# Kernel optimization log

Measured on AMD Instinct MI355X. Metric: run time of the kernel, lower is better.

The kernel has to match this reference:

```python
import jax, jax.numpy as jnp
import numpy as np

NUM_QUESTION = 10000


def setup_inputs() -> dict:
    key = jax.random.key(0)
    ks = jax.random.split(key, 12)
    B, L, DK, SLOTS = 64, 200, 128, 64
    return {
        "question_seq": jax.random.randint(ks[0], (B, L), 0, NUM_QUESTION),
        "correct_seq": jax.random.randint(ks[1], (B, L), 0, 2),
        "q_emb": jax.random.normal(ks[2], (NUM_QUESTION, DK), jnp.float32) * 0.05,
        "v_emb": jax.random.normal(ks[3], (2 * NUM_QUESTION, DK), jnp.float32) * 0.05,
        "Mk": jax.random.normal(ks[4], (SLOTS, DK), jnp.float32) * 0.1,
        "Mv0": jax.random.normal(ks[5], (SLOTS, DK), jnp.float32) * 0.1,
        "eW": jax.random.normal(ks[6], (DK, DK), jnp.float32) * 0.05,
        "eb": jnp.zeros((DK,), jnp.float32),
        "aW": jax.random.normal(ks[7], (DK, DK), jnp.float32) * 0.05,
        "ab": jnp.zeros((DK,), jnp.float32),
        "fW": jax.random.normal(ks[8], (DK, 2 * DK), jnp.float32) * 0.05,
        "fb": jnp.zeros((DK,), jnp.float32),
        "pW": jax.random.normal(ks[9], (1, DK), jnp.float32) * 0.05,
        "pb": jnp.zeros((1,), jnp.float32),
    }


def reference(question_seq, correct_seq, q_emb, v_emb, Mk, Mv0,
              eW, eb, aW, ab, fW, fb, pW, pb):
    B = question_seq.shape[0]
    x = question_seq + NUM_QUESTION * correct_seq          # [B, L]
    k = q_emb[question_seq]                                # [B, L, DK]
    v = v_emb[x]                                           # [B, L, DK]
    w = jax.nn.softmax(jnp.einsum("bld,sd->bls", k, Mk), axis=-1)  # [B, L, S]
    e = jax.nn.sigmoid(v @ eW.T + eb)                      # [B, L, DK]
    a = jnp.tanh(v @ aW.T + ab)                            # [B, L, DK]

    Mv_init = jnp.broadcast_to(Mv0[None], (B,) + Mv0.shape)  # [B, S, DK]

    def step(Mvt, inp):
        wt, et, at = inp  # [B,S], [B,DK], [B,DK]
        # read uses memory BEFORE the write (Mv[:, :-1] in the original)
        read = jnp.einsum("bs,bsd->bd", wt, Mvt)
        we = wt[:, :, None]
        Mvt = Mvt * (1.0 - we * et[:, None, :]) + we * at[:, None, :]
        return Mvt, read

    xs = (w.transpose(1, 0, 2), e.transpose(1, 0, 2), a.transpose(1, 0, 2))
    _, reads = jax.lax.scan(step, Mv_init, xs)             # reads: [L, B, DK]
    reads = reads.transpose(1, 0, 2)                       # [B, L, DK]

    f = jnp.tanh(jnp.concatenate([reads, k], axis=-1) @ fW.T + fb)
    predict_score = jax.nn.sigmoid(f @ pW.T + pb)[..., 0]  # [B, L]
    return predict_score
```

## Files before the change

kernel.cpp:

```cpp
#include <hip/hip_runtime.h>
#include <hip/hip_bf16.h>

#define NQ 10000
#define BATCH 64
#define SEQL 200
#define DKD 128
#define SLOTS 64
#define NTOK (BATCH*SEQL)

typedef __attribute__((ext_vector_type(8))) short bh8;
typedef __attribute__((ext_vector_type(4))) float f32x4;
typedef unsigned short u16;
typedef unsigned int u32;

__device__ __forceinline__ float sigmoidf_(float x){ return 1.0f/(1.0f + __expf(-x)); }
__device__ __forceinline__ float tanhf_(float x){
  float ax = fminf(fabsf(x), 30.0f);
  float t = __expf(-2.0f*ax);
  float r = (1.0f-t)/(1.0f+t);
  return copysignf(r, x);
}
__device__ __forceinline__ u16 f2b(float x){
  u32 u = __builtin_bit_cast(u32, x);
  u32 r = (u + 0x7FFFu + ((u >> 16) & 1u)) >> 16;
  return (u16)r;
}
__device__ __forceinline__ bh8 cvt8(const float* s){
  float4 v0 = *(const float4*)s, v1 = *(const float4*)(s + 4);
  bh8 h;
  h[0]=(short)f2b(v0.x); h[1]=(short)f2b(v0.y); h[2]=(short)f2b(v0.z); h[3]=(short)f2b(v0.w);
  h[4]=(short)f2b(v1.x); h[5]=(short)f2b(v1.y); h[6]=(short)f2b(v1.z); h[7]=(short)f2b(v1.w);
  return h;
}
__device__ __forceinline__ int swz(int row, int col16, int rowBytes){
  return row*rowBytes + ((col16 ^ (row & 7)) << 4);
}

__global__ __launch_bounds__(512) void wea_kernel(
    const int* __restrict__ qseq, const int* __restrict__ cseq,
    const float* __restrict__ q_emb, const float* __restrict__ v_emb,
    const float* __restrict__ Mk, const float* __restrict__ eW,
    const float* __restrict__ aW,
    const float* __restrict__ eb, const float* __restrict__ ab,
    float* __restrict__ w_out, float* __restrict__ eT, float* __restrict__ aT)
{
  __shared__ __align__(16) char smem[73728];
  char* As = smem;
  char* Bs = smem + 8192;
  float* Ls = (float*)(smem + 24576);

  const int tid = threadIdx.x;
  const int l = tid & 63, wv = tid >> 6;
  const bool isW = (blockIdx.x < 400);
  const int tok0 = (isW ? blockIdx.x : blockIdx.x - 400) * 32;

  {
    int row = tid >> 4, c16 = tid & 15;
    const float* src;
    if (isW){ int q = qseq[tok0+row]; src = q_emb + (size_t)q*DKD + c16*8; }
    else    { int x = qseq[tok0+row] + NQ*cseq[tok0+row]; src = v_emb + (size_t)x*DKD + c16*8; }
    *(bh8*)(As + swz(row, c16, 256)) = cvt8(src);
  }
  if (isW){
    #pragma unroll
    for (int m = 0; m < 2; ++m){
      int idx = tid + 512*m; int row = idx >> 4, c16 = idx & 15;
      *(bh8*)(Bs + swz(row, c16, 256)) = cvt8(Mk + (size_t)row*DKD + c16*8);
    }
  } else {
    #pragma unroll
    for (int m = 0; m < 8; ++m){
      int idx = tid + 512*m; int row = idx >> 4, c16 = idx & 15;
      const float* src = (row < 128) ? (eW + (size_t)row*DKD) : (aW + (size_t)(row-128)*DKD);
      *(bh8*)(Bs + swz(row, c16, 256)) = cvt8(src + c16*8);
    }
  }
  __syncthreads();

  if (isW){
    const int m = wv & 1, n = wv >> 1;
    f32x4 acc = {0.f,0.f,0.f,0.f};
    #pragma unroll
    for (int kc = 0; kc < 4; ++kc){
      bh8 af = *(const bh8*)(As + swz(m*16 + (l&15), kc*4 + (l>>4), 256));
      bh8 bf = *(const bh8*)(Bs + swz(n*16 + (l&15), kc*4 + (l>>4), 256));
      acc = __builtin_amdgcn_mfma_f32_16x16x32_bf16(af, bf, acc, 0, 0, 0);
    }
    #pragma unroll
    for (int r = 0; r < 4; ++r){
      int tok = m*16 + (l>>4)*4 + r, out = n*16 + (l&15);
      Ls[tok*68 + out] = acc[r];
    }
    __syncthreads();
    #pragma unroll
    for (int i = 0; i < 4; ++i){
      int tok = wv*4 + i;
      float x = Ls[tok*68 + l];
      float mx = x;
      #pragma unroll
      for (int off = 32; off >= 1; off >>= 1) mx = fmaxf(mx, __shfl_xor(mx, off));
      float p = __expf(x - mx);
      float s = p;
      #pragma unroll
      for (int off = 32; off >= 1; off >>= 1) s += __shfl_xor(s, off);
      w_out[(size_t)(tok0+tok)*SLOTS + l] = p / s;
    }
  } else {
    const int m = wv & 1, nq = (wv >> 1) * 4;
    f32x4 acc[4] = {{0.f,0.f,0.f,0.f},{0.f,0.f,0.f,0.f},{0.f,0.f,0.f,0.f},{0.f,0.f,0.f,0.f}};
    #pragma unroll
    for (int kc = 0; kc < 4; ++kc){
      bh8 af = *(const bh8*)(As + swz(m*16 + (l&15), kc*4 + (l>>4), 256));
      #pragma unroll
      for (int j = 0; j < 4; ++j){
        bh8 bf = *(const bh8*)(Bs + swz((nq+j)*16 + (l&15), kc*4 + (l>>4), 256));
        acc[j] = __builtin_amdgcn_mfma_f32_16x16x32_bf16(af, bf, acc[j], 0, 0, 0);
      }
    }
    #pragma unroll
    for (int j = 0; j < 4; ++j){
      int out = (nq+j)*16 + (l&15);
      bool is_e = (out < 128);
      int dd = out & 127;
      float bias = is_e ? eb[dd] : ab[dd];
      float4 sv;
      #pragma unroll
      for (int r = 0; r < 4; ++r){
        float xv = acc[j][r] + bias;
        ((float*)&sv)[r] = is_e ? sigmoidf_(xv) : tanhf_(xv);
      }
      int tg = tok0 + m*16 + (l>>4)*4;
      int bb = tg / SEQL, tl = tg - bb*SEQL;
      float* dst = (is_e ? eT : aT) + ((size_t)bb*DKD + dd)*SEQL + tl;
      *(float4*)dst = sv;
    }
  }
}

__device__ __forceinline__ float dpp_row_sum16(float x){
  float t;
  t = __builtin_bit_cast(float, __builtin_amdgcn_update_dpp(0, __builtin_bit_cast(int,x), 0x111, 0xf, 0xf, true)); x += t;
  t = __builtin_bit_cast(float, __builtin_amdgcn_update_dpp(0, __builtin_bit_cast(int,x), 0x112, 0xf, 0xf, true)); x += t;
  t = __builtin_bit_cast(float, __builtin_amdgcn_update_dpp(0, __builtin_bit_cast(int,x), 0x114, 0xf, 0xf, true)); x += t;
  t = __builtin_bit_cast(float, __builtin_amdgcn_update_dpp(0, __builtin_bit_cast(int,x), 0x118, 0xf, 0xf, true)); x += t;
  return x;
}

#define TCH 8
#define NCH 25

__global__ __launch_bounds__(256) void scan_kernel(
    const float* __restrict__ Mv0,
    const float* __restrict__ w_in, const float* __restrict__ eT,
    const float* __restrict__ aT, u16* __restrict__ r16)
{
  __shared__ float eaS[2][2][16][8];
  __shared__ float rbuf[2][TCH][16];
  const int tid = threadIdx.x;
  const int b  = blockIdx.x >> 3;
  const int d0 = (blockIdx.x & 7) << 4;
  const int c  = tid >> 4;
  const int g  = tid & 15;
  const int d  = d0 + c;
  const bool wlane = (g == 15);

  float mv0 = Mv0[(4*g+0)*DKD + d];
  float mv1 = Mv0[(4*g+1)*DKD + d];
  float mv2 = Mv0[(4*g+2)*DKD + d];
  float mv3 = Mv0[(4*g+3)*DKD + d];

  const float4* wsrc = (const float4*)(w_in + (size_t)b*SEQL*SLOTS);
  const int sdd = (tid & 127) >> 3, sth = tid & 7;
  const float* easrc = ((tid < 128) ? eT : aT) + ((size_t)b*DKD + d0 + sdd)*SEQL + sth;
  const int sarr = (tid < 128) ? 1 : 0;
  u16* rp = r16 + (size_t)b*SEQL*DKD + d0;

  float4 wA[TCH], wB[TCH];

  {
    #pragma unroll
    for (int i = 0; i < TCH; ++i) wA[i] = wsrc[i*16 + g];
    float ea0 = easrc[0];
    eaS[0][(tid < 128) ? 0 : 1][sdd][sth] = ea0;
    __syncthreads();
  }

  #define COMPUTE(P, WC)                                                  \
    _Pragma("unroll")                                                     \
    for (int u = 0; u < 2; ++u){                                          \
      float eq[4], aq[4];                                                 \
      *(float4*)eq = *(const float4*)&eaS[P][0][c][u*4];                  \
      *(float4*)aq = *(const float4*)&eaS[P][1][c][u*4];                  \
      _Pragma("unroll")                                                   \
      for (int v = 0; v < 4; ++v){                                        \
        const int tt = u*4 + v;                                           \
        float4 wq = WC[tt];                                               \
        float r = wq.x*mv0; r = fmaf(wq.y, mv1, r);                       \
        r = fmaf(wq.z, mv2, r); r = fmaf(wq.w, mv3, r);                   \
        r = dpp_row_sum16(r);                                             \
        if (wlane) rbuf[P][tt][c] = r;                                    \
        const float ev = eq[v], av = aq[v];                               \
        mv0 = fmaf(wq.x, fmaf(-mv0, ev, av), mv0);                        \
        mv1 = fmaf(wq.y, fmaf(-mv1, ev, av), mv1);                        \
        mv2 = fmaf(wq.z, fmaf(-mv2, ev, av), mv2);                        \
        mv3 = fmaf(wq.w, fmaf(-mv3, ev, av), mv3);                        \
      }                                                                   \
    }

  #define STORER(CK, P)                                                  \
    if (tid < 64){                                                       \
      int t = tid >> 3, dp = tid & 7;                                    \
      float2 rv = *(const float2*)&rbuf[P][t][dp*2];                     \
      u32 pk = (u32)f2b(rv.x) | ((u32)f2b(rv.y) << 16);                  \
      *(u32*)(rp + (size_t)((CK)*TCH + t)*DKD + dp*2) = pk;              \
    }

  #define PHASE(CK, P, WC, WN)                                           \
    {                                                                    \
      if ((CK) > 0) STORER((CK)-1, (P)^1);                               \
      const int T0n = ((CK)+1)*TCH;                                      \
      _Pragma("unroll")                                                  \
      for (int i = 0; i < TCH; ++i) WN[i] = wsrc[(T0n+i)*16 + g];        \
      float ean = easrc[T0n];                                            \
      COMPUTE(P, WC)                                                     \
      eaS[(P)^1][(tid < 128) ? 0 : 1][sdd][sth] = ean;                   \
      __syncthreads();                                                   \
    }

  for (int ck = 0; ck < 24; ck += 2){
    PHASE(ck,   0, wA, wB)
    PHASE(ck+1, 1, wB, wA)
  }
  STORER(23, 1);
  COMPUTE(0, wA)
  __syncthreads();
  STORER(24, 0);

  #undef COMPUTE
  #undef STORER
  #undef PHASE
  (void)sarr;
}

__global__ __launch_bounds__(512) void p3_kernel(
    const int* __restrict__ qseq, const float* __restrict__ q_emb,
    const u16* __restrict__ r16, const float* __restrict__ fW,
    const float* __restrict__ fb, const float* __restrict__ pW,
    const float* __restrict__ pb, float* __restrict__ out)
{
  __shared__ __align__(16) char smem[81920];
  char* As = smem;
  char* Bs = smem + 16384;

  const int tid = threadIdx.x;
  const int l = tid & 63, wv = tid >> 6;
  const int tok0 = blockIdx.x * 32;

  #pragma unroll
  for (int m = 0; m < 2; ++m){
    int idx = tid + 512*m; int row = idx >> 5, c16 = idx & 31;
    bh8 v;
    if (c16 < 16){
      v = *(const bh8*)(r16 + (size_t)(tok0+row)*DKD + c16*8);
    } else {
      int q = qseq[tok0+row];
      v = cvt8(q_emb + (size_t)q*DKD + (c16-16)*8);
    }
    *(bh8*)(As + swz(row, c16, 512)) = v;
  }
  #pragma unroll
  for (int m = 0; m < 8; ++m){
    int idx = tid + 512*m; int row = idx >> 5, c16 = idx & 31;
    *(bh8*)(Bs + swz(row, c16, 512)) = cvt8(fW + (size_t)row*256 + c16*8);
  }
  __syncthreads();

  const int m = wv & 1, np = (wv >> 1) * 2;
  f32x4 acc[2] = {{0.f,0.f,0.f,0.f},{0.f,0.f,0.f,0.f}};
  #pragma unroll
  for (int kc = 0; kc < 8; ++kc){
    bh8 af = *(const bh8*)(As + swz(m*16 + (l&15), kc*4 + (l>>4), 512));
    #pragma unroll
    for (int j = 0; j < 2; ++j){
      bh8 bf = *(const bh8*)(Bs + swz((np+j)*16 + (l&15), kc*4 + (l>>4), 512));
      acc[j] = __builtin_amdgcn_mfma_f32_16x16x32_bf16(af, bf, acc[j], 0, 0, 0);
    }
  }
  float pp[4] = {0.f,0.f,0.f,0.f};
  #pragma unroll
  for (int j = 0; j < 2; ++j){
    int o = (np+j)*16 + (l&15);
    float bias = fb[o], pw = pW[o];
    #pragma unroll
    for (int r = 0; r < 4; ++r){
      float f = tanhf_(acc[j][r] + bias);
      pp[r] = fmaf(f, pw, pp[r]);
    }
  }
  #pragma unroll
  for (int r = 0; r < 4; ++r){
    pp[r] += __shfl_xor(pp[r], 1);
    pp[r] += __shfl_xor(pp[r], 2);
    pp[r] += __shfl_xor(pp[r], 4);
    pp[r] += __shfl_xor(pp[r], 8);
  }
  __syncthreads();
  float* pbuf = (float*)smem;
  if ((l & 15) == 0){
    #pragma unroll
    for (int r = 0; r < 4; ++r){
      int tok = m*16 + (l>>4)*4 + r;
      pbuf[wv*32 + tok] = pp[r];
    }
  }
  __syncthreads();
  if (tid < 32){
    int mm = tid >> 4;
    float s = pbuf[(mm+0)*32 + tid] + pbuf[(mm+2)*32 + tid]
            + pbuf[(mm+4)*32 + tid] + pbuf[(mm+6)*32 + tid];
    out[tok0 + tid] = sigmoidf_(s + pb[0]);
  }
}

extern "C" void kernel_launch(void* const* d_in, const int* in_sizes, int n_in,
                              void* d_out, int out_size, void* d_ws, size_t ws_size,
                              hipStream_t stream) {
  const int*   qseq  = (const int*)d_in[0];
  const int*   cseq  = (const int*)d_in[1];
  const float* q_emb = (const float*)d_in[2];
  const float* v_emb = (const float*)d_in[3];
  const float* Mk    = (const float*)d_in[4];
  const float* Mv0   = (const float*)d_in[5];
  const float* eW    = (const float*)d_in[6];
  const float* eb    = (const float*)d_in[7];
  const float* aW    = (const float*)d_in[8];
  const float* ab    = (const float*)d_in[9];
  const float* fW    = (const float*)d_in[10];
  const float* fb    = (const float*)d_in[11];
  const float* pW    = (const float*)d_in[12];
  const float* pb    = (const float*)d_in[13];

  char* ws = (char*)d_ws;
  float* w_buf = (float*)ws;
  float* eT    = (float*)(ws + 3276800);
  float* aT    = (float*)(ws + 9830400);
  u16*   r16   = (u16*)  (ws + 16384000);
  float* outp  = (float*)d_out;

  hipLaunchKernelGGL(wea_kernel, dim3(800), dim3(512), 0, stream,
                     qseq, cseq, q_emb, v_emb, Mk, eW, aW, eb, ab,
                     w_buf, eT, aT);
  hipLaunchKernelGGL(scan_kernel, dim3(512), dim3(256), 0, stream,
                     Mv0, w_buf, eT, aT, r16);
  hipLaunchKernelGGL(p3_kernel, dim3(NTOK/32), dim3(512), 0, stream,
                     qseq, q_emb, r16, fW, fb, pW, pb, outp);
}
```

Measured before the change: 50.62 us.

## Transpose softmax weights to time-major and drop LDS staging in scan kernel

The wea kernel now writes the softmax attention weights in a per-batch, slot-major, time-contiguous layout, matching how e and a are already stored. The scan kernel then loads w, e and a for 4 timesteps straight into registers with vector loads, prefetched three chunks deep. This removes the shared-memory staging buffers and the per-chunk __syncthreads, and the lane that owns each column writes the read results directly instead of going through a shared buffer. The cost is more global load instructions per thread, since every lane fetches its own e/a values, and narrow 2-byte strided stores for r16.

```diff
diff --git a/kernel.cpp b/kernel.cpp
--- a/kernel.cpp
+++ b/kernel.cpp
@@ -42,7 +42,7 @@
     const float* __restrict__ Mk, const float* __restrict__ eW,
     const float* __restrict__ aW,
     const float* __restrict__ eb, const float* __restrict__ ab,
-    float* __restrict__ w_out, float* __restrict__ eT, float* __restrict__ aT)
+    float* __restrict__ wT, float* __restrict__ eT, float* __restrict__ aT)
 {
   __shared__ __align__(16) char smem[73728];
   char* As = smem;
@@ -92,6 +92,7 @@
       Ls[tok*68 + out] = acc[r];
     }
     __syncthreads();
+    f32x4 ps;
     #pragma unroll
     for (int i = 0; i < 4; ++i){
       int tok = wv*4 + i;
@@ -103,8 +104,11 @@
       float s = p;
       #pragma unroll
       for (int off = 32; off >= 1; off >>= 1) s += __shfl_xor(s, off);
-      w_out[(size_t)(tok0+tok)*SLOTS + l] = p / s;
-    }
+      ps[i] = p / s;
+    }
+    int tg = tok0 + wv*4;
+    int bb = tg / SEQL, tl = tg - bb*SEQL;
+    *(f32x4*)(wT + ((size_t)bb*SLOTS + l)*SEQL + tl) = ps;
   } else {
     const int m = wv & 1, nq = (wv >> 1) * 4;
     f32x4 acc[4] = {{0.f,0.f,0.f,0.f},{0.f,0.f,0.f,0.f},{0.f,0.f,0.f,0.f},{0.f,0.f,0.f,0.f}};
@@ -123,16 +127,16 @@
       bool is_e = (out < 128);
       int dd = out & 127;
       float bias = is_e ? eb[dd] : ab[dd];
-      float4 sv;
+      f32x4 sv;
       #pragma unroll
       for (int r = 0; r < 4; ++r){
         float xv = acc[j][r] + bias;
-        ((float*)&sv)[r] = is_e ? sigmoidf_(xv) : tanhf_(xv);
+        sv[r] = is_e ? sigmoidf_(xv) : tanhf_(xv);
       }
       int tg = tok0 + m*16 + (l>>4)*4;
       int bb = tg / SEQL, tl = tg - bb*SEQL;
       float* dst = (is_e ? eT : aT) + ((size_t)bb*DKD + dd)*SEQL + tl;
-      *(float4*)dst = sv;
+      *(f32x4*)dst = sv;
     }
   }
 }
@@ -146,100 +150,79 @@
   return x;
 }
 
-#define TCH 8
-#define NCH 25
+#define SCH 4
+#define SNCH 50
 
 __global__ __launch_bounds__(256) void scan_kernel(
     const float* __restrict__ Mv0,
-    const float* __restrict__ w_in, const float* __restrict__ eT,
-    const float* __restrict__ aT, u16* __restrict__ r16)
+    const float* __restrict__ wT,
+    const float* __restrict__ eT,
+    const float* __restrict__ aT,
+    u16* __restrict__ r16)
 {
-  __shared__ float eaS[2][2][16][8];
-  __shared__ float rbuf[2][TCH][16];
   const int tid = threadIdx.x;
   const int b  = blockIdx.x >> 3;
   const int d0 = (blockIdx.x & 7) << 4;
   const int c  = tid >> 4;
   const int g  = tid & 15;
   const int d  = d0 + c;
-  const bool wlane = (g == 15);
+  const bool wl = (g == 15);
 
   float mv0 = Mv0[(4*g+0)*DKD + d];
   float mv1 = Mv0[(4*g+1)*DKD + d];
   float mv2 = Mv0[(4*g+2)*DKD + d];
   float mv3 = Mv0[(4*g+3)*DKD + d];
 
-  const float4* wsrc = (const float4*)(w_in + (size_t)b*SEQL*SLOTS);
-  const int sdd = (tid & 127) >> 3, sth = tid & 7;
-  const float* easrc = ((tid < 128) ? eT : aT) + ((size_t)b*DKD + d0 + sdd)*SEQL + sth;
-  const int sarr = (tid < 128) ? 1 : 0;
-  u16* rp = r16 + (size_t)b*SEQL*DKD + d0;
-
-  float4 wA[TCH], wB[TCH];
-
-  {
-    #pragma unroll
-    for (int i = 0; i < TCH; ++i) wA[i] = wsrc[i*16 + g];
-    float ea0 = easrc[0];
-    eaS[0][(tid < 128) ? 0 : 1][sdd][sth] = ea0;
-    __syncthreads();
-  }
-
-  #define COMPUTE(P, WC)                                                  \
+  const float* wbase = wT + ((size_t)b*SLOTS + 4*g)*SEQL;
+  const float* ebase = eT + ((size_t)b*DKD + d)*SEQL;
+  const float* abase = aT + ((size_t)b*DKD + d)*SEQL;
+  u16* rp = r16 + (size_t)b*SEQL*DKD + d;
+
+  f32x4 Aw0,Aw1,Aw2,Aw3,Ae,Aa;
+  f32x4 Bw0,Bw1,Bw2,Bw3,Be,Ba;
+  f32x4 Cw0,Cw1,Cw2,Cw3,Ce,Ca;
+
+  #define LOADS(S, CK) { const int t0_ = (CK)*SCH;                        \
+    S##w0 = *(const f32x4*)(wbase + 0*SEQL + t0_);                        \
+    S##w1 = *(const f32x4*)(wbase + 1*SEQL + t0_);                        \
+    S##w2 = *(const f32x4*)(wbase + 2*SEQL + t0_);                        \
+    S##w3 = *(const f32x4*)(wbase + 3*SEQL + t0_);                        \
+    S##e  = *(const f32x4*)(ebase + t0_);                                 \
+    S##a  = *(const f32x4*)(abase + t0_); }
+
+  #define CHUNK(S, CK) {                                                  \
+    float rr[SCH];                                                        \
     _Pragma("unroll")                                                     \
-    for (int u = 0; u < 2; ++u){                                          \
-      float eq[4], aq[4];                                                 \
-      *(float4*)eq = *(const float4*)&eaS[P][0][c][u*4];                  \
-      *(float4*)aq = *(const float4*)&eaS[P][1][c][u*4];                  \
+    for (int v = 0; v < SCH; ++v){                                        \
+      const float w0 = S##w0[v], w1 = S##w1[v], w2 = S##w2[v], w3 = S##w3[v]; \
+      float r = w0*mv0; r = fmaf(w1, mv1, r);                             \
+      r = fmaf(w2, mv2, r); r = fmaf(w3, mv3, r);                         \
+      rr[v] = dpp_row_sum16(r);                                           \
+      const float ev = S##e[v], av = S##a[v];                             \
+      mv0 = fmaf(w0, fmaf(-mv0, ev, av), mv0);                            \
+      mv1 = fmaf(w1, fmaf(-mv1, ev, av), mv1);                            \
+      mv2 = fmaf(w2, fmaf(-mv2, ev, av), mv2);                            \
+      mv3 = fmaf(w3, fmaf(-mv3, ev, av), mv3);                            \
+    }                                                                     \
+    if (wl){                                                              \
       _Pragma("unroll")                                                   \
-      for (int v = 0; v < 4; ++v){                                        \
-        const int tt = u*4 + v;                                           \
-        float4 wq = WC[tt];                                               \
-        float r = wq.x*mv0; r = fmaf(wq.y, mv1, r);                       \
-        r = fmaf(wq.z, mv2, r); r = fmaf(wq.w, mv3, r);                   \
-        r = dpp_row_sum16(r);                                             \
-        if (wlane) rbuf[P][tt][c] = r;                                    \
-        const float ev = eq[v], av = aq[v];                               \
-        mv0 = fmaf(wq.x, fmaf(-mv0, ev, av), mv0);                        \
-        mv1 = fmaf(wq.y, fmaf(-mv1, ev, av), mv1);                        \
-        mv2 = fmaf(wq.z, fmaf(-mv2, ev, av), mv2);                        \
-        mv3 = fmaf(wq.w, fmaf(-mv3, ev, av), mv3);                        \
-      }                                                                   \
-    }
-
-  #define STORER(CK, P)                                                  \
-    if (tid < 64){                                                       \
-      int t = tid >> 3, dp = tid & 7;                                    \
-      float2 rv = *(const float2*)&rbuf[P][t][dp*2];                     \
-      u32 pk = (u32)f2b(rv.x) | ((u32)f2b(rv.y) << 16);                  \
-      *(u32*)(rp + (size_t)((CK)*TCH + t)*DKD + dp*2) = pk;              \
-    }
-
-  #define PHASE(CK, P, WC, WN)                                           \
-    {                                                                    \
-      if ((CK) > 0) STORER((CK)-1, (P)^1);                               \
-      const int T0n = ((CK)+1)*TCH;                                      \
-      _Pragma("unroll")                                                  \
-      for (int i = 0; i < TCH; ++i) WN[i] = wsrc[(T0n+i)*16 + g];        \
-      float ean = easrc[T0n];                                            \
-      COMPUTE(P, WC)                                                     \
-      eaS[(P)^1][(tid < 128) ? 0 : 1][sdd][sth] = ean;                   \
-      __syncthreads();                                                   \
-    }
-
-  for (int ck = 0; ck < 24; ck += 2){
-    PHASE(ck,   0, wA, wB)
-    PHASE(ck+1, 1, wB, wA)
-  }
-  STORER(23, 1);
-  COMPUTE(0, wA)
-  __syncthreads();
-  STORER(24, 0);
-
-  #undef COMPUTE
-  #undef STORER
-  #undef PHASE
-  (void)sarr;
+      for (int v = 0; v < SCH; ++v)                                       \
+        rp[(size_t)((CK)*SCH + v)*DKD] = f2b(rr[v]);                      \
+    } }
+
+  LOADS(A, 0)
+  LOADS(B, 1)
+  #pragma unroll 1
+  for (int m = 0; m < 16; ++m){
+    const int ck = 3*m;
+    LOADS(C, ck+2)  CHUNK(A, ck)
+    LOADS(A, ck+3)  CHUNK(B, ck+1)
+    LOADS(B, ck+4)  CHUNK(C, ck+2)
+  }
+  CHUNK(A, 48)
+  CHUNK(B, 49)
+  #undef LOADS
+  #undef CHUNK
 }
 
 __global__ __launch_bounds__(512) void p3_kernel(
@@ -341,7 +324,7 @@
   const float* pb    = (const float*)d_in[13];
 
   char* ws = (char*)d_ws;
-  float* w_buf = (float*)ws;
+  float* wT    = (float*)ws;
   float* eT    = (float*)(ws + 3276800);
   float* aT    = (float*)(ws + 9830400);
   u16*   r16   = (u16*)  (ws + 16384000);
@@ -349,9 +332,9 @@
 
   hipLaunchKernelGGL(wea_kernel, dim3(800), dim3(512), 0, stream,
                      qseq, cseq, q_emb, v_emb, Mk, eW, aW, eb, ab,
-                     w_buf, eT, aT);
+                     wT, eT, aT);
   hipLaunchKernelGGL(scan_kernel, dim3(512), dim3(256), 0, stream,
-                     Mv0, w_buf, eT, aT, r16);
+                     Mv0, wT, eT, aT, r16);
   hipLaunchKernelGGL(p3_kernel, dim3(NTOK/32), dim3(512), 0, stream,
                      qseq, q_emb, r16, fW, fb, pW, pb, outp);
 }
```

Measured after the change: 80.03 us. 58.1% more time.
